# Optimization experiments

Hardware: AMD Instinct MI355X
Metric: run time of the kernel (lower is better)

Reference implementation:

```python
import jax, jax.numpy as jnp
import numpy as np

B, N, G = 16, 6000, 512
NUM_PAD_GT = 64  # zero-padded gt rows per image


def _make_boxes(key, shape):
    # sample two corner points and sort so (y1,x1) <= (y2,x2)
    r = jax.random.uniform(key, shape[:-1] + (4,), dtype=jnp.float32)
    lo = jnp.minimum(r[..., :2], r[..., 2:])
    hi = jnp.maximum(r[..., :2], r[..., 2:])
    return jnp.concatenate([lo, hi], axis=-1)


def setup_inputs() -> dict:
    key = jax.random.key(0)
    k1, k2, k3 = jax.random.split(key, 3)
    rois = _make_boxes(k1, (B, N, 4))
    gt_boxes = _make_boxes(k2, (B, G, 4))
    # zero-pad tail gt rows (remove_zero_padding signal)
    gt_boxes = gt_boxes.at[:, G - NUM_PAD_GT:, :].set(0.0)
    # ids in [-2, 18]: <0 crowd, ==0 padding, >0 real classes
    gt_ids = jax.random.randint(k3, (B, G), 0, 21, dtype=jnp.int64) - 2
    gt_ids = jnp.where(jnp.arange(G) >= G - NUM_PAD_GT, 0, gt_ids)
    return {"rois": rois, "gt_ids": gt_ids, "gt_boxes": gt_boxes}


def _pairwise_iou(boxes1, boxes2):
    # boxes1: [B,N,4], boxes2: [B,G,4] in (y1,x1,y2,x2) -> IoU [B,N,G]
    b1 = boxes1[:, :, None, :]  # [B,N,1,4]
    b2 = boxes2[:, None, :, :]  # [B,1,G,4]
    y1 = jnp.maximum(b1[..., 0], b2[..., 0])
    x1 = jnp.maximum(b1[..., 1], b2[..., 1])
    y2 = jnp.minimum(b1[..., 2], b2[..., 2])
    x2 = jnp.minimum(b1[..., 3], b2[..., 3])
    inter = jnp.maximum(y2 - y1, 0.0) * jnp.maximum(x2 - x1, 0.0)
    area1 = (b1[..., 2] - b1[..., 0]) * (b1[..., 3] - b1[..., 1])
    area2 = (b2[..., 2] - b2[..., 0]) * (b2[..., 3] - b2[..., 1])
    union = area1 + area2 - inter
    return inter / (union + 1e-8)


def reference(rois, gt_ids, gt_boxes):
    # remove_zero_padding -> validity masks (jit-friendly: mask instead of gather)
    valid_roi = jnp.sum(jnp.abs(rois), axis=-1) > 0.0      # [B,N]
    valid_gt = jnp.sum(jnp.abs(gt_boxes), axis=-1) > 0.0   # [B,G]
    crowd = valid_gt & (gt_ids < 0)                          # [B,G]
    non_crowd = valid_gt & (gt_ids > 0)                      # [B,G]

    iou = _pairwise_iou(rois, gt_boxes)                      # [B,N,G]
    # max IoU against non-crowd / crowd gt subsets (masked cols -> 0, IoU >= 0)
    iou_nc_max = jnp.max(jnp.where(non_crowd[:, None, :], iou, 0.0), axis=2)
    iou_c_max = jnp.max(jnp.where(crowd[:, None, :], iou, 0.0), axis=2)
    iou_nc_max = jnp.where(valid_roi, iou_nc_max, 0.0)       # [B,N]
    iou_c_max = jnp.where(valid_roi, iou_c_max, 0.0)

    positive_mask = valid_roi & (iou_nc_max >= 0.5)
    negative_mask = valid_roi & (iou_nc_max < 0.5) & (iou_c_max < 1e-3)

    iou_maxes = jnp.stack([iou_nc_max, iou_c_max], axis=1)   # [B,2,N]
    return iou_maxes, positive_mask, negative_mask
```

## Files before the change

### kernel.cpp

```cpp
#include <hip/hip_runtime.h>

#define BB 16
#define NN 6000
#define GG 512
#define WAVES 8
#define RPT 3
#define RPB (RPT * 64)

__global__ __launch_bounds__(64 * WAVES) void det_kernel(
    const float4* __restrict__ rois,
    const int*    __restrict__ gt_ids,
    const float4* __restrict__ gt_boxes,
    float*        __restrict__ out)
{
    __shared__ float4 s_box[GG];
    __shared__ float4 s_area4[GG / 4];
    __shared__ float  s_ncm[WAVES][RPB];
    __shared__ float  s_cm[WAVES][RPB];
    __shared__ float  s_val[RPB];
    __shared__ int    s_wn[WAVES], s_wc[WAVES];
    float* s_area = (float*)s_area4;

    const int b    = blockIdx.y;
    const int tid  = threadIdx.x;
    const int wave = tid >> 6;
    const int lane = tid & 63;

    const int nbase = blockIdx.x * RPB;
    float4 r[RPT];
    float  rs[RPT];
    #pragma unroll
    for (int i = 0; i < RPT; ++i) {
        int n = nbase + i * 64 + lane;
        r[i] = (n < NN) ? rois[b * NN + n] : make_float4(0.f, 0.f, 0.f, 0.f);
    }
    const float4 box = gt_boxes[b * GG + tid];
    const int    id  = gt_ids[b * GG + tid];

    #pragma unroll
    for (int i = 0; i < RPT; ++i) {
        rs[i] = (r[i].z - r[i].x) * (r[i].w - r[i].y) + 1e-8f;
        if (wave == 0)
            s_val[i * 64 + lane] =
                ((fabsf(r[i].x) + fabsf(r[i].y) + fabsf(r[i].z) + fabsf(r[i].w)) > 0.f) ? 1.f : 0.f;
    }

    const float asum = fabsf(box.x) + fabsf(box.y) + fabsf(box.z) + fabsf(box.w);
    const bool pn = (asum > 0.0f) && (id > 0);
    const bool pc = (asum > 0.0f) && (id < 0);
    const unsigned long long mn = __ballot(pn);
    const unsigned long long mc = __ballot(pc);
    if (lane == 0) { s_wn[wave] = __popcll(mn); s_wc[wave] = __popcll(mc); }
    __syncthreads();

    int bn = 0, bc = 0, ncnt = 0, ccnt = 0;
    #pragma unroll
    for (int w = 0; w < WAVES; ++w) {
        int pw = s_wn[w], cw = s_wc[w];
        if (w < wave) { bn += pw; bc += cw; }
        ncnt += pw; ccnt += cw;
    }
    const int lo     = GG - ccnt;
    int nc_eff = (ncnt + 3) & ~3;
    int lo_pad = lo & ~3;
    if (nc_eff > lo_pad) nc_eff = lo_pad;

    {
        const unsigned long long lt = (1ULL << lane) - 1ULL;
        if (pn) {
            int idx = bn + __popcll(mn & lt);
            s_box[idx]  = box;
            s_area[idx] = (box.z - box.x) * (box.w - box.y);
        }
        if (pc) {
            int idx = (GG - 1) - (bc + __popcll(mc & lt));
            s_box[idx]  = box;
            s_area[idx] = (box.z - box.x) * (box.w - box.y);
        }
        const float4 z = make_float4(0.f, 0.f, 0.f, 0.f);
        if (tid < 4) {
            int i = ncnt + tid;
            if (i < nc_eff) { s_box[i] = z; s_area[i] = 0.f; }
        } else if (tid < 8) {
            int i = lo_pad + (tid - 4);
            if (i < lo) { s_box[i] = z; s_area[i] = 0.f; }
        }
    }
    __syncthreads();

    auto tval = [](const float4& rr, float rsum, const float4& g4, float ga) -> float {
        float dy = fminf(rr.z, g4.z) - fmaxf(rr.x, g4.x);
        float dx = fminf(rr.w, g4.w) - fmaxf(rr.y, g4.y);
        float inter = fmaxf(fmaxf(dy, 0.f) * dx, 0.f);
        return inter * __builtin_amdgcn_rcpf(rsum + ga);
    };

    float anc[RPT] = {0.f, 0.f, 0.f};
    float ac[RPT]  = {0.f, 0.f, 0.f};

    auto run = [&](int q0, int q1, float* acc) {
        if (q0 >= q1) return;
        float4 nb0 = s_box[4 * q0 + 0];
        float4 nb1 = s_box[4 * q0 + 1];
        float4 nb2 = s_box[4 * q0 + 2];
        float4 nb3 = s_box[4 * q0 + 3];
        float4 na  = s_area4[q0];
        #pragma unroll 2
        for (int q = q0; q < q1; ++q) {
            const float4 cb0 = nb0, cb1 = nb1, cb2 = nb2, cb3 = nb3, ca = na;
            const int qn = (q + 1 < q1) ? q + 1 : q0;
            nb0 = s_box[4 * qn + 0];
            nb1 = s_box[4 * qn + 1];
            nb2 = s_box[4 * qn + 2];
            nb3 = s_box[4 * qn + 3];
            na  = s_area4[qn];
            #pragma unroll
            for (int i = 0; i < RPT; ++i) {
                float t0 = tval(r[i], rs[i], cb0, ca.x);
                float t1 = tval(r[i], rs[i], cb1, ca.y);
                float t2 = tval(r[i], rs[i], cb2, ca.z);
                float t3 = tval(r[i], rs[i], cb3, ca.w);
                acc[i] = fmaxf(acc[i], fmaxf(fmaxf(t0, t1), fmaxf(t2, t3)));
            }
        }
    };

    {
        const int ngr = nc_eff >> 2;
        const int gpw = (ngr + WAVES - 1) / WAVES;
        const int q0 = __builtin_amdgcn_readfirstlane(wave * gpw);
        const int q1 = __builtin_amdgcn_readfirstlane(min(ngr, q0 + gpw));
        run(q0, q1, anc);
    }
    {
        const int cg0 = lo_pad >> 2;
        const int cgn = (GG >> 2) - cg0;
        const int gpw = (cgn + WAVES - 1) / WAVES;
        const int q0 = __builtin_amdgcn_readfirstlane(cg0 + wave * gpw);
        const int q1 = __builtin_amdgcn_readfirstlane(min(GG >> 2, q0 + gpw));
        run(q0, q1, ac);
    }

    #pragma unroll
    for (int i = 0; i < RPT; ++i) {
        s_ncm[wave][i * 64 + lane] = anc[i];
        s_cm[wave][i * 64 + lane]  = ac[i];
    }
    __syncthreads();

    if (tid < RPB) {
        const int n = nbase + tid;
        if (n < NN) {
            float a = s_ncm[0][tid], c = s_cm[0][tid];
            #pragma unroll
            for (int w = 1; w < WAVES; ++w) {
                a = fmaxf(a, s_ncm[w][tid]);
                c = fmaxf(c, s_cm[w][tid]);
            }
            const float vr = s_val[tid];
            a *= vr;
            c *= vr;
            const float nc_max = a * __builtin_amdgcn_rcpf(1.f - a);
            const float c_max  = c * __builtin_amdgcn_rcpf(1.f - c);

            out[b * 2 * NN + n]      = nc_max;
            out[b * 2 * NN + NN + n] = c_max;
            const float pos = (vr > 0.f && nc_max >= 0.5f) ? 1.0f : 0.0f;
            const float neg = (vr > 0.f && nc_max < 0.5f && c_max < 0.001f) ? 1.0f : 0.0f;
            out[BB * 2 * NN + b * NN + n]           = pos;
            out[BB * 2 * NN + BB * NN + b * NN + n] = neg;
        }
    }
}

extern "C" void kernel_launch(void* const* d_in, const int* in_sizes, int n_in,
                              void* d_out, int out_size, void* d_ws, size_t ws_size,
                              hipStream_t stream) {
    const float4* rois     = (const float4*)d_in[0];
    const int*    gt_ids   = (const int*)d_in[1];
    const float4* gt_boxes = (const float4*)d_in[2];
    float*        out      = (float*)d_out;

    dim3 grid((NN + RPB - 1) / RPB, BB);
    det_kernel<<<grid, 64 * WAVES, 0, stream>>>(rois, gt_ids, gt_boxes, out);
}
```

Measured before the change: 23.79 us.

## Double waves and rows per thread, interleave GT groups across waves

Raises the block to 16 waves with 6 ROIs per thread so each LDS GT load is reused over more ROIs and the grid roughly matches the CU count. GT compaction stays on the first 8 waves, and GT groups are now assigned to waves round-robin instead of in contiguous chunks. This adds register pressure and a larger shared reduction buffer, and may leave waves idle on the small crowd subset.

```diff
diff --git a/kernel.cpp b/kernel.cpp
--- a/kernel.cpp
+++ b/kernel.cpp
@@ -3,9 +3,11 @@
 #define BB 16
 #define NN 6000
 #define GG 512
-#define WAVES 8
-#define RPT 3
+#define WAVES 16
+#define RPT 6
 #define RPB (RPT * 64)
+
+__device__ __forceinline__ int rfl(int v) { return __builtin_amdgcn_readfirstlane(v); }
 
 __global__ __launch_bounds__(64 * WAVES) void det_kernel(
     const float4* __restrict__ rois,
@@ -18,7 +20,7 @@
     __shared__ float  s_ncm[WAVES][RPB];
     __shared__ float  s_cm[WAVES][RPB];
     __shared__ float  s_val[RPB];
-    __shared__ int    s_wn[WAVES], s_wc[WAVES];
+    __shared__ int    s_wn[8], s_wc[8];
     float* s_area = (float*)s_area4;
 
     const int b    = blockIdx.y;
@@ -34,9 +36,6 @@
         int n = nbase + i * 64 + lane;
         r[i] = (n < NN) ? rois[b * NN + n] : make_float4(0.f, 0.f, 0.f, 0.f);
     }
-    const float4 box = gt_boxes[b * GG + tid];
-    const int    id  = gt_ids[b * GG + tid];
-
     #pragma unroll
     for (int i = 0; i < RPT; ++i) {
         rs[i] = (r[i].z - r[i].x) * (r[i].w - r[i].y) + 1e-8f;
@@ -45,27 +44,34 @@
                 ((fabsf(r[i].x) + fabsf(r[i].y) + fabsf(r[i].z) + fabsf(r[i].w)) > 0.f) ? 1.f : 0.f;
     }
 
-    const float asum = fabsf(box.x) + fabsf(box.y) + fabsf(box.z) + fabsf(box.w);
-    const bool pn = (asum > 0.0f) && (id > 0);
-    const bool pc = (asum > 0.0f) && (id < 0);
-    const unsigned long long mn = __ballot(pn);
-    const unsigned long long mc = __ballot(pc);
-    if (lane == 0) { s_wn[wave] = __popcll(mn); s_wc[wave] = __popcll(mc); }
+    bool pn = false, pc = false;
+    float4 box;
+    unsigned long long mn = 0, mc = 0;
+    if (wave < 8) {
+        box = gt_boxes[b * GG + tid];
+        const int id = gt_ids[b * GG + tid];
+        const float asum = fabsf(box.x) + fabsf(box.y) + fabsf(box.z) + fabsf(box.w);
+        pn = (asum > 0.0f) && (id > 0);
+        pc = (asum > 0.0f) && (id < 0);
+        mn = __ballot(pn);
+        mc = __ballot(pc);
+        if (lane == 0) { s_wn[wave] = __popcll(mn); s_wc[wave] = __popcll(mc); }
+    }
     __syncthreads();
 
     int bn = 0, bc = 0, ncnt = 0, ccnt = 0;
     #pragma unroll
-    for (int w = 0; w < WAVES; ++w) {
+    for (int w = 0; w < 8; ++w) {
         int pw = s_wn[w], cw = s_wc[w];
         if (w < wave) { bn += pw; bc += cw; }
         ncnt += pw; ccnt += cw;
     }
-    const int lo     = GG - ccnt;
+    const int lo = GG - ccnt;
     int nc_eff = (ncnt + 3) & ~3;
     int lo_pad = lo & ~3;
     if (nc_eff > lo_pad) nc_eff = lo_pad;
 
-    {
+    if (wave < 8) {
         const unsigned long long lt = (1ULL << lane) - 1ULL;
         if (pn) {
             int idx = bn + __popcll(mn & lt);
@@ -77,6 +83,8 @@
             s_box[idx]  = box;
             s_area[idx] = (box.z - box.x) * (box.w - box.y);
         }
+    }
+    {
         const float4 z = make_float4(0.f, 0.f, 0.f, 0.f);
         if (tid < 4) {
             int i = ncnt + tid;
@@ -95,20 +103,19 @@
         return inter * __builtin_amdgcn_rcpf(rsum + ga);
     };
 
-    float anc[RPT] = {0.f, 0.f, 0.f};
-    float ac[RPT]  = {0.f, 0.f, 0.f};
+    float anc[RPT] = {0.f, 0.f, 0.f, 0.f, 0.f, 0.f};
+    float ac[RPT]  = {0.f, 0.f, 0.f, 0.f, 0.f, 0.f};
 
-    auto run = [&](int q0, int q1, float* acc) {
-        if (q0 >= q1) return;
+    auto run = [&](int q0, int qend, float* acc) {
+        if (q0 >= qend) return;
         float4 nb0 = s_box[4 * q0 + 0];
         float4 nb1 = s_box[4 * q0 + 1];
         float4 nb2 = s_box[4 * q0 + 2];
         float4 nb3 = s_box[4 * q0 + 3];
         float4 na  = s_area4[q0];
-        #pragma unroll 2
-        for (int q = q0; q < q1; ++q) {
+        for (int q = q0; q < qend; q += WAVES) {
             const float4 cb0 = nb0, cb1 = nb1, cb2 = nb2, cb3 = nb3, ca = na;
-            const int qn = (q + 1 < q1) ? q + 1 : q0;
+            const int qn = (q + WAVES < qend) ? q + WAVES : q0;
             nb0 = s_box[4 * qn + 0];
             nb1 = s_box[4 * qn + 1];
             nb2 = s_box[4 * qn + 2];
@@ -126,19 +133,12 @@
     };
 
     {
-        const int ngr = nc_eff >> 2;
-        const int gpw = (ngr + WAVES - 1) / WAVES;
-        const int q0 = __builtin_amdgcn_readfirstlane(wave * gpw);
-        const int q1 = __builtin_amdgcn_readfirstlane(min(ngr, q0 + gpw));
-        run(q0, q1, anc);
+        const int ngr = rfl(nc_eff >> 2);
+        run(wave, ngr, anc);
     }
     {
-        const int cg0 = lo_pad >> 2;
-        const int cgn = (GG >> 2) - cg0;
-        const int gpw = (cgn + WAVES - 1) / WAVES;
-        const int q0 = __builtin_amdgcn_readfirstlane(cg0 + wave * gpw);
-        const int q1 = __builtin_amdgcn_readfirstlane(min(GG >> 2, q0 + gpw));
-        run(q0, q1, ac);
+        const int cg0 = rfl(lo_pad >> 2);
+        run(cg0 + wave, GG >> 2, ac);
     }
 
     #pragma unroll
```

Result: slower. 25.20 us (+5.9%).
